# Kernel tuning notes

Measured on AMD Instinct MI355X. Metric: run time of the kernel, lower is better.

## Reference

```python
import jax, jax.numpy as jnp
import numpy as np
from jax import lax

FEAT = 384        # features
FFN = 768         # ffn_features (chunk=True -> halves of 384)
ZDIM = FFN // 2   # 384
HID = 192         # AE hidden
B, N = 4, 128
LN_EPS = 1e-5


def gelu(x):
    return jax.nn.gelu(x, approximate=False)  # torch nn.GELU default = exact erf


def setup_inputs() -> dict:
    key = jax.random.key(0)
    ks = jax.random.split(key, 12)

    def lin(k, fan_in, shape):
        bound = 1.0 / np.sqrt(fan_in)
        return jax.random.uniform(k, shape, jnp.float32, -bound, bound)

    return {
        "x": jax.random.normal(ks[0], (B, N, FEAT), jnp.float32),
        "U_w": lin(ks[1], FEAT, (FEAT, FFN)),
        "U_b": lin(ks[2], FEAT, (FFN,)),
        "ln_w": jnp.ones((ZDIM,), jnp.float32),
        "ln_b": jnp.zeros((ZDIM,), jnp.float32),
        "enc_w": lin(ks[3], ZDIM, (ZDIM, HID)),
        "enc_b": lin(ks[4], ZDIM, (HID,)),
        "dec_w": lin(ks[5], HID, (HID, ZDIM)),
        "dec_b": lin(ks[6], HID, (ZDIM,)),
        "V_w": lin(ks[7], ZDIM, (ZDIM, FEAT)),
        "V_b": lin(ks[8], ZDIM, (FEAT,)),
    }


def _ae(z, enc_w, enc_b, dec_w, dec_b):
    h = gelu(z @ enc_w + enc_b)
    return h @ dec_w + dec_b


def reference(x, U_w, U_b, ln_w, ln_b, enc_w, enc_b, dec_w, dec_b, V_w, V_b):
    h = gelu(x @ U_w + U_b)                    # (B,N,FFN)
    xh, z = jnp.split(h, 2, axis=-1)           # chunk=True: (B,N,ZDIM) each
    z = lax.stop_gradient(z)                   # z.detach()
    mu = jnp.mean(z, axis=-1, keepdims=True)
    var = jnp.var(z, axis=-1, keepdims=True)
    z = (z - mu) / jnp.sqrt(var + LN_EPS) * ln_w + ln_b

    n = z.shape[1]
    eye = jnp.eye(n, dtype=z.dtype)
    # z_mask[b,i,j,:] = z[b,j,:] if i==j else 0   (mask_type='zeros')
    z_mask = eye[None, :, :, None] * z[:, None, :, :]   # (B,N,N,ZDIM)
    preds = _ae(z_mask, enc_w, enc_b, dec_w, dec_b)      # (B,N,N,ZDIM)
    dist = jnp.einsum('bijf,bjf->bij', preds, z)         # (B,N,N)
    attn = lax.stop_gradient(jax.nn.softmax(dist, axis=-1))
    out = jnp.einsum('bij,bjf->bif', attn, xh)           # (B,N,ZDIM)
    return out @ V_w + V_b                               # (B,N,FEAT)
```

## Files before the change

### kernel.cpp

```cpp
#include <hip/hip_runtime.h>
#include <hip/hip_bf16.h>
#include <math.h>

#define FEAT 384
#define FFN  768
#define ZDIM 384
#define HID  192
#define BB   4
#define NN   128
#define BN   (BB*NN)

__device__ __forceinline__ float gelu_exact(float x) {
    return 0.5f * x * (1.0f + erff(x * 0.70710678118654752440f));
}

__device__ __forceinline__ float bflo(unsigned u) { return __uint_as_float(u << 16); }
__device__ __forceinline__ float bfhi(unsigned u) { return __uint_as_float(u & 0xFFFF0000u); }

template<bool F32>
__device__ __forceinline__ float ldg(const void* p, int i) {
    if constexpr (F32) return ((const float*)p)[i];
    return __uint_as_float(((unsigned)((const unsigned short*)p)[i]) << 16);
}

__device__ __forceinline__ unsigned pack2(float a, float b) {
    __hip_bfloat16 ba = __float2bfloat16(a), bb = __float2bfloat16(b);
    unsigned short ua, ub;
    __builtin_memcpy(&ua, &ba, 2);
    __builtin_memcpy(&ub, &bb, 2);
    return (unsigned)ua | ((unsigned)ub << 16);
}

template<bool F32>
__device__ __forceinline__ void st8(void* p, size_t off, const float v[8]) {
    if constexpr (F32) {
        *(float4*)((float*)p + off)     = make_float4(v[0], v[1], v[2], v[3]);
        *(float4*)((float*)p + off + 4) = make_float4(v[4], v[5], v[6], v[7]);
    } else {
        uint4 u;
        u.x = pack2(v[0], v[1]); u.y = pack2(v[2], v[3]);
        u.z = pack2(v[4], v[5]); u.w = pack2(v[6], v[7]);
        *(uint4*)((unsigned short*)p + off) = u;
    }
}

template<bool F32> struct V8;
template<> struct V8<true> {
    float4 a, b;
    __device__ __forceinline__ void load(const void* p, size_t off) {
        a = *(const float4*)((const float*)p + off);
        b = *(const float4*)((const float*)p + off + 4);
    }
    __device__ __forceinline__ float g(int i) const {
        return (i < 4) ? (&a.x)[i] : (&b.x)[i - 4];
    }
};
template<> struct V8<false> {
    uint4 u;
    __device__ __forceinline__ void load(const void* p, size_t off) {
        u = *(const uint4*)((const unsigned short*)p + off);
    }
    __device__ __forceinline__ float g(int i) const {
        const unsigned w = (&u.x)[i >> 1];
        return (i & 1) ? bfhi(w) : bflo(w);
    }
};
template<bool F32> struct V4;
template<> struct V4<true> {
    float4 a;
    __device__ __forceinline__ void load(const void* p, size_t off) {
        a = *(const float4*)((const float*)p + off);
    }
    __device__ __forceinline__ float g(int i) const { return (&a.x)[i]; }
};
template<> struct V4<false> {
    uint2 u;
    __device__ __forceinline__ void load(const void* p, size_t off) {
        u = *(const uint2*)((const unsigned short*)p + off);
    }
    __device__ __forceinline__ float g(int i) const {
        const unsigned w = (&u.x)[i >> 1];
        return (i & 1) ? bfhi(w) : bflo(w);
    }
};

__device__ __forceinline__ bool is_f32(const void* ln_w) {
    return ((const unsigned short*)ln_w)[0] == 0;
}

__device__ __forceinline__ float block_sum(float v, float* sm) {
    for (int o = 32; o > 0; o >>= 1) v += __shfl_down(v, o, 64);
    const int lane = threadIdx.x & 63, w = threadIdx.x >> 6;
    __syncthreads();
    if (lane == 0) sm[w] = v;
    __syncthreads();
    return sm[0] + sm[1] + sm[2] + sm[3] + sm[4] + sm[5];
}
__device__ __forceinline__ float2 block_sum2(float vx, float vy, float* sm) {
    for (int o = 32; o > 0; o >>= 1) {
        vx += __shfl_down(vx, o, 64);
        vy += __shfl_down(vy, o, 64);
    }
    const int lane = threadIdx.x & 63, w = threadIdx.x >> 6;
    __syncthreads();
    if (lane == 0) { sm[w] = vx; sm[w + 6] = vy; }
    __syncthreads();
    return make_float2(sm[0] + sm[1] + sm[2] + sm[3] + sm[4] + sm[5],
                       sm[6] + sm[7] + sm[8] + sm[9] + sm[10] + sm[11]);
}
__device__ __forceinline__ float block_max(float v, float* sm) {
    for (int o = 32; o > 0; o >>= 1) v = fmaxf(v, __shfl_down(v, o, 64));
    const int lane = threadIdx.x & 63, w = threadIdx.x >> 6;
    __syncthreads();
    if (lane == 0) sm[w] = v;
    __syncthreads();
    return fmaxf(fmaxf(fmaxf(sm[0], sm[1]), fmaxf(sm[2], sm[3])), fmaxf(sm[4], sm[5]));
}

template<bool F32>
__device__ void rows_body(
    const void* __restrict__ x, const void* __restrict__ U_w,
    const void* __restrict__ U_b, const void* __restrict__ ln_w,
    const void* __restrict__ ln_b, const void* __restrict__ enc_w,
    const void* __restrict__ enc_b, const void* __restrict__ dec_w,
    const void* __restrict__ dec_b,
    float* __restrict__ xh, float* __restrict__ d0, float* __restrict__ diag)
{
    const int r0 = 2 * blockIdx.x, r1 = r0 + 1;
    const int t = threadIdx.x;
    __shared__ float xs[2][FEAT];
    __shared__ float zs[2][ZDIM];
    __shared__ float hid[2][HID];
    __shared__ float gh[HID];
    __shared__ float part[4608];
    __shared__ float sm[12];

    xs[0][t] = ldg<F32>(x, r0 * FEAT + t);
    xs[1][t] = ldg<F32>(x, r1 * FEAT + t);
    if (t < HID) gh[t] = gelu_exact(ldg<F32>(enc_b, t));
    __syncthreads();

    const int cg = t % 96, kh = t / 96;
    const int cU = 8 * cg;
    const int kb = 96 * kh;
    float acc0[8] = {0,0,0,0,0,0,0,0}, acc1[8] = {0,0,0,0,0,0,0,0};
    {
        V8<F32> wa[8], wb[8];
        #pragma unroll
        for (int j = 0; j < 8; j++) wa[j].load(U_w, (size_t)(kb + j) * FFN + cU);
        for (int k0 = kb; k0 < kb + 96; k0 += 16) {
            #pragma unroll
            for (int j = 0; j < 8; j++) wb[j].load(U_w, (size_t)(k0 + 8 + j) * FFN + cU);
            #pragma unroll
            for (int j = 0; j < 8; j++) {
                const float x0 = xs[0][k0 + j], x1 = xs[1][k0 + j];
                #pragma unroll
                for (int i = 0; i < 8; i++) {
                    const float w = wa[j].g(i);
                    acc0[i] = fmaf(x0, w, acc0[i]);
                    acc1[i] = fmaf(x1, w, acc1[i]);
                }
            }
            if (k0 + 16 < kb + 96) {
                #pragma unroll
                for (int j = 0; j < 8; j++) wa[j].load(U_w, (size_t)(k0 + 16 + j) * FFN + cU);
            }
            #pragma unroll
            for (int j = 0; j < 8; j++) {
                const float x0 = xs[0][k0 + 8 + j], x1 = xs[1][k0 + 8 + j];
                #pragma unroll
                for (int i = 0; i < 8; i++) {
                    const float w = wb[j].g(i);
                    acc0[i] = fmaf(x0, w, acc0[i]);
                    acc1[i] = fmaf(x1, w, acc1[i]);
                }
            }
        }
    }
    if (kh > 0) {
        float* p = &part[(kh - 1) * 1536 + cg];
        #pragma unroll
        for (int i = 0; i < 8; i++) { p[i * 96] = acc0[i]; p[768 + i * 96] = acc1[i]; }
    }
    __syncthreads();

    float h0[8], h1[8];
    float s1a = 0.f, s1b = 0.f, s2a = 0.f, s2b = 0.f;
    if (kh == 0) {
        #pragma unroll
        for (int i = 0; i < 8; i++) {
            const float ub = ldg<F32>(U_b, cU + i);
            float v0 = acc0[i] + ub, v1 = acc1[i] + ub;
            #pragma unroll
            for (int kk = 0; kk < 3; kk++) {
                v0 += part[kk * 1536 + i * 96 + cg];
                v1 += part[kk * 1536 + 768 + i * 96 + cg];
            }
            v0 = gelu_exact(v0); v1 = gelu_exact(v1);
            h0[i] = v0; h1[i] = v1;
            if (cg >= 48) { s1a += v0; s2a += v0 * v0; s1b += v1; s2b += v1 * v1; }
        }
        if (cg < 48) {
            *(float4*)(xh + (size_t)r0 * ZDIM + cU)     = make_float4(h0[0], h0[1], h0[2], h0[3]);
            *(float4*)(xh + (size_t)r0 * ZDIM + cU + 4) = make_float4(h0[4], h0[5], h0[6], h0[7]);
            *(float4*)(xh + (size_t)r1 * ZDIM + cU)     = make_float4(h1[0], h1[1], h1[2], h1[3]);
            *(float4*)(xh + (size_t)r1 * ZDIM + cU + 4) = make_float4(h1[4], h1[5], h1[6], h1[7]);
        }
    }

    const float2 S1 = block_sum2(s1a, s1b, sm);
    const float2 S2 = block_sum2(s2a, s2b, sm);
    const float mu0 = S1.x * (1.0f / ZDIM), mu1 = S1.y * (1.0f / ZDIM);
    const float rs0 = rsqrtf(S2.x * (1.0f / ZDIM) - mu0 * mu0 + 1e-5f);
    const float rs1 = rsqrtf(S2.y * (1.0f / ZDIM) - mu1 * mu1 + 1e-5f);
    if (kh == 0 && cg >= 48) {
        #pragma unroll
        for (int i = 0; i < 8; i++) {
            const int zc = cU - ZDIM + i;
            const float w = ldg<F32>(ln_w, zc), bb = ldg<F32>(ln_b, zc);
            zs[0][zc] = (h0[i] - mu0) * rs0 * w + bb;
            zs[1][zc] = (h1[i] - mu1) * rs1 * w + bb;
        }
    }
    __syncthreads();

    {
        const int cgE = t % 48, khE = t / 48;
        const int cE = 4 * cgE, kbE = 48 * khE;
        float e0a[4] = {0,0,0,0}, e1a[4] = {0,0,0,0};
        V4<F32> va[8], vb[8];
        #pragma unroll
        for (int j = 0; j < 8; j++) va[j].load(enc_w, (size_t)(kbE + j) * HID + cE);
        for (int k0 = kbE; k0 < kbE + 48; k0 += 16) {
            #pragma unroll
            for (int j = 0; j < 8; j++) vb[j].load(enc_w, (size_t)(k0 + 8 + j) * HID + cE);
            #pragma unroll
            for (int j = 0; j < 8; j++) {
                const float z0 = zs[0][k0 + j], z1 = zs[1][k0 + j];
                #pragma unroll
                for (int i = 0; i < 4; i++) {
                    const float w = va[j].g(i);
                    e0a[i] = fmaf(z0, w, e0a[i]);
                    e1a[i] = fmaf(z1, w, e1a[i]);
                }
            }
            if (k0 + 16 < kbE + 48) {
                #pragma unroll
                for (int j = 0; j < 8; j++) va[j].load(enc_w, (size_t)(k0 + 16 + j) * HID + cE);
            }
            #pragma unroll
            for (int j = 0; j < 8; j++) {
                const float z0 = zs[0][k0 + 8 + j], z1 = zs[1][k0 + 8 + j];
                #pragma unroll
                for (int i = 0; i < 4; i++) {
                    const float w = vb[j].g(i);
                    e0a[i] = fmaf(z0, w, e0a[i]);
                    e1a[i] = fmaf(z1, w, e1a[i]);
                }
            }
        }
        if (khE > 0) {
            float* p = &part[(khE - 1) * 384 + cgE];
            #pragma unroll
            for (int i = 0; i < 4; i++) { p[i * 48] = e0a[i]; p[192 + i * 48] = e1a[i]; }
        }
        __syncthreads();
        if (khE == 0) {
            #pragma unroll
            for (int i = 0; i < 4; i++) {
                const float ebv = ldg<F32>(enc_b, cE + i);
                float v0 = e0a[i] + ebv, v1 = e1a[i] + ebv;
                #pragma unroll
                for (int kk = 0; kk < 7; kk++) {
                    v0 += part[kk * 384 + i * 48 + cgE];
                    v1 += part[kk * 384 + 192 + i * 48 + cgE];
                }
                hid[0][cE + i] = gelu_exact(v0);
                hid[1][cE + i] = gelu_exact(v1);
            }
        }
        __syncthreads();
    }

    {
        const int cgD = t % 96, khD = t / 96;
        const int cD = 4 * cgD, kbD = 48 * khD;
        float aa[4] = {0,0,0,0}, ab_[4] = {0,0,0,0}, ac[4] = {0,0,0,0};
        V4<F32> va[8], vb[8];
        #pragma unroll
        for (int j = 0; j < 8; j++) va[j].load(dec_w, (size_t)(kbD + j) * ZDIM + cD);
        for (int k0 = kbD; k0 < kbD + 48; k0 += 16) {
            #pragma unroll
            for (int j = 0; j < 8; j++) vb[j].load(dec_w, (size_t)(k0 + 8 + j) * ZDIM + cD);
            #pragma unroll
            for (int j = 0; j < 8; j++) {
                const float v0 = hid[0][k0 + j], v1 = hid[1][k0 + j], gv = gh[k0 + j];
                #pragma unroll
                for (int i = 0; i < 4; i++) {
                    const float w = va[j].g(i);
                    aa[i] = fmaf(v0, w, aa[i]);
                    ab_[i] = fmaf(v1, w, ab_[i]);
                    ac[i] = fmaf(gv, w, ac[i]);
                }
            }
            if (k0 + 16 < kbD + 48) {
                #pragma unroll
                for (int j = 0; j < 8; j++) va[j].load(dec_w, (size_t)(k0 + 16 + j) * ZDIM + cD);
            }
            #pragma unroll
            for (int j = 0; j < 8; j++) {
                const float v0 = hid[0][k0 + 8 + j], v1 = hid[1][k0 + 8 + j], gv = gh[k0 + 8 + j];
                #pragma unroll
                for (int i = 0; i < 4; i++) {
                    const float w = vb[j].g(i);
                    aa[i] = fmaf(v0, w, aa[i]);
                    ab_[i] = fmaf(v1, w, ab_[i]);
                    ac[i] = fmaf(gv, w, ac[i]);
                }
            }
        }
        if (khD > 0) {
            float* p = &part[(khD - 1) * 1152 + cgD];
            #pragma unroll
            for (int i = 0; i < 4; i++) {
                p[i * 96] = aa[i];
                p[384 + i * 96] = ab_[i];
                p[768 + i * 96] = ac[i];
            }
        }
        __syncthreads();
        float pd0 = 0.f, pd1 = 0.f, pe0 = 0.f, pe1 = 0.f;
        if (khD == 0) {
            #pragma unroll
            for (int i = 0; i < 4; i++) {
                const int c = cD + i;
                const float dbv = ldg<F32>(dec_b, c);
                float v0 = aa[i] + dbv, v1 = ab_[i] + dbv, v2 = ac[i] + dbv;
                #pragma unroll
                for (int kk = 0; kk < 3; kk++) {
                    v0 += part[kk * 1152 + i * 96 + cgD];
                    v1 += part[kk * 1152 + 384 + i * 96 + cgD];
                    v2 += part[kk * 1152 + 768 + i * 96 + cgD];
                }
                const float z0 = zs[0][c], z1 = zs[1][c];
                pd0 = fmaf(v0, z0, pd0);
                pd1 = fmaf(v1, z1, pd1);
                pe0 = fmaf(v2, z0, pe0);
                pe1 = fmaf(v2, z1, pe1);
            }
        }
        const float2 DG = block_sum2(pd0, pd1, sm);
        const float2 DD = block_sum2(pe0, pe1, sm);
        if (t == 0) {
            diag[r0] = DG.x; diag[r1] = DG.y;
            d0[r0] = DD.x;   d0[r1] = DD.y;
        }
    }
}

__global__ __launch_bounds__(384) void k_rows(
    const void* x, const void* U_w, const void* U_b,
    const void* ln_w, const void* ln_b,
    const void* enc_w, const void* enc_b,
    const void* dec_w, const void* dec_b,
    float* xh, float* d0, float* diag)
{
    if (is_f32(ln_w))
        rows_body<true >(x, U_w, U_b, ln_w, ln_b, enc_w, enc_b, dec_w, dec_b, xh, d0, diag);
    else
        rows_body<false>(x, U_w, U_b, ln_w, ln_b, enc_w, enc_b, dec_w, dec_b, xh, d0, diag);
}

template<bool F32>
__device__ void out_body(
    const float* __restrict__ d0, const float* __restrict__ diag,
    const float* __restrict__ xh,
    const void* __restrict__ V_w, const void* __restrict__ V_b,
    void* __restrict__ out)
{
    const int r0 = 2 * blockIdx.x, r1 = r0 + 1;
    const int b = r0 >> 7;
    const int t = threadIdx.x;
    __shared__ float e0s[NN];
    __shared__ float as[2][ZDIM];
    __shared__ float pv[5376];
    __shared__ float sm[12];

    float d0v = -INFINITY, dgv = -INFINITY;
    if (t < NN) { d0v = d0[b * NN + t]; dgv = diag[b * NN + t]; }
    const float m = block_max(fmaxf(d0v, dgv), sm);
    float e0v = 0.f;
    if (t < NN) { e0v = expf(d0v - m); e0s[t] = e0v; }
    const float S = block_sum(e0v, sm);

    const float e00 = expf(d0[r0] - m), e01 = expf(d0[r1] - m);
    const float ed0 = expf(diag[r0] - m), ed1 = expf(diag[r1] - m);
    const float inv0 = 1.0f / (S - e00 + ed0);
    const float inv1 = 1.0f / (S - e01 + ed1);

    float acc = 0.f;
    {
        const float* xp = xh + (size_t)b * NN * ZDIM + t;
        float wa[16], wb[16];
        #pragma unroll
        for (int j = 0; j < 16; j++) wa[j] = xp[(size_t)j * ZDIM];
        for (int j0 = 0; j0 < NN; j0 += 32) {
            #pragma unroll
            for (int j = 0; j < 16; j++) wb[j] = xp[(size_t)(j0 + 16 + j) * ZDIM];
            #pragma unroll
            for (int j = 0; j < 16; j++) acc = fmaf(e0s[j0 + j], wa[j], acc);
            if (j0 + 32 < NN) {
                #pragma unroll
                for (int j = 0; j < 16; j++) wa[j] = xp[(size_t)(j0 + 32 + j) * ZDIM];
            }
            #pragma unroll
            for (int j = 0; j < 16; j++) acc = fmaf(e0s[j0 + 16 + j], wb[j], acc);
        }
    }
    as[0][t] = (acc + (ed0 - e00) * xh[(size_t)r0 * ZDIM + t]) * inv0;
    as[1][t] = (acc + (ed1 - e01) * xh[(size_t)r1 * ZDIM + t]) * inv1;
    __syncthreads();

    const int cg = t % 48, kh = t / 48;
    const int cV = 8 * cg, kb = 48 * kh;
    float a0[8] = {0,0,0,0,0,0,0,0}, a1[8] = {0,0,0,0,0,0,0,0};
    {
        V8<F32> va[8], vb[8];
        #pragma unroll
        for (int j = 0; j < 8; j++) va[j].load(V_w, (size_t)(kb + j) * FEAT + cV);
        for (int f0 = kb; f0 < kb + 48; f0 += 16) {
            #pragma unroll
            for (int j = 0; j < 8; j++) vb[j].load(V_w, (size_t)(f0 + 8 + j) * FEAT + cV);
            #pragma unroll
            for (int j = 0; j < 8; j++) {
                const float s0 = as[0][f0 + j], s1 = as[1][f0 + j];
                #pragma unroll
                for (int i = 0; i < 8; i++) {
                    const float w = va[j].g(i);
                    a0[i] = fmaf(s0, w, a0[i]);
                    a1[i] = fmaf(s1, w, a1[i]);
                }
            }
            if (f0 + 16 < kb + 48) {
                #pragma unroll
                for (int j = 0; j < 8; j++) va[j].load(V_w, (size_t)(f0 + 16 + j) * FEAT + cV);
            }
            #pragma unroll
            for (int j = 0; j < 8; j++) {
                const float s0 = as[0][f0 + 8 + j], s1 = as[1][f0 + 8 + j];
                #pragma unroll
                for (int i = 0; i < 8; i++) {
                    const float w = vb[j].g(i);
                    a0[i] = fmaf(s0, w, a0[i]);
                    a1[i] = fmaf(s1, w, a1[i]);
                }
            }
        }
    }
    if (kh > 0) {
        float* p = &pv[(kh - 1) * 768 + cg];
        #pragma unroll
        for (int i = 0; i < 8; i++) { p[i * 48] = a0[i]; p[384 + i * 48] = a1[i]; }
    }
    __syncthreads();
    if (kh == 0) {
        float o0[8], o1[8];
        #pragma unroll
        for (int i = 0; i < 8; i++) {
            const float vb_ = ldg<F32>(V_b, cV + i);
            float u0 = a0[i] + vb_, u1 = a1[i] + vb_;
            #pragma unroll
            for (int kk = 0; kk < 7; kk++) {
                u0 += pv[kk * 768 + i * 48 + cg];
                u1 += pv[kk * 768 + 384 + i * 48 + cg];
            }
            o0[i] = u0; o1[i] = u1;
        }
        st8<F32>(out, (size_t)r0 * FEAT + cV, o0);
        st8<F32>(out, (size_t)r1 * FEAT + cV, o1);
    }
}

__global__ __launch_bounds__(384) void k_out(
    const void* ln_w,
    const float* d0, const float* diag, const float* xh,
    const void* V_w, const void* V_b, void* out)
{
    if (is_f32(ln_w))
        out_body<true >(d0, diag, xh, V_w, V_b, out);
    else
        out_body<false>(d0, diag, xh, V_w, V_b, out);
}

extern "C" void kernel_launch(void* const* d_in, const int* in_sizes, int n_in,
                              void* d_out, int out_size, void* d_ws, size_t ws_size,
                              hipStream_t stream) {
    const void* x     = d_in[0];
    const void* U_w   = d_in[1];
    const void* U_b   = d_in[2];
    const void* ln_w  = d_in[3];
    const void* ln_b  = d_in[4];
    const void* enc_w = d_in[5];
    const void* enc_b = d_in[6];
    const void* dec_w = d_in[7];
    const void* dec_b = d_in[8];
    const void* V_w   = d_in[9];
    const void* V_b   = d_in[10];

    float* ws   = (float*)d_ws;
    float* xh   = ws;
    float* d0   = xh + (size_t)BN * ZDIM;
    float* diag = d0 + BN;

    k_rows<<<BN / 2, 384, 0, stream>>>(x, U_w, U_b, ln_w, ln_b, enc_w, enc_b,
                                       dec_w, dec_b, xh, d0, diag);
    k_out<<<BN / 2, 384, 0, stream>>>(ln_w, d0, diag, xh, V_w, V_b, d_out);
}
```

Baseline: 111.2 us.

## Apply V projection to xh before attention and split row blocks by FFN half

Because out = attn·xh·V_w and the attention here is a rank-structured softmax (a shared baseline plus a diagonal correction), the V_w projection is moved ahead of attention. Each token's xh is projected to Y = xh·V_w inside the rows kernel, and the final kernel only forms the per-batch weighted sum of Y and applies the per-row diagonal correction. The rows kernel now launches two blocks per row pair: one computes the xh half and the Y projection, the other the z half with layernorm and the autoencoder. This raises parallelism and removes the per-row-pair V_w GEMM from the second kernel. The combine kernel runs only 16 blocks, which may leave most of the GPU idle, and the bf16 output now uses scalar stores.

```diff
diff --git a/kernel.cpp b/kernel.cpp
--- a/kernel.cpp
+++ b/kernel.cpp
@@ -22,26 +22,10 @@
     if constexpr (F32) return ((const float*)p)[i];
     return __uint_as_float(((unsigned)((const unsigned short*)p)[i]) << 16);
 }
-
-__device__ __forceinline__ unsigned pack2(float a, float b) {
-    __hip_bfloat16 ba = __float2bfloat16(a), bb = __float2bfloat16(b);
-    unsigned short ua, ub;
-    __builtin_memcpy(&ua, &ba, 2);
-    __builtin_memcpy(&ub, &bb, 2);
-    return (unsigned)ua | ((unsigned)ub << 16);
-}
-
 template<bool F32>
-__device__ __forceinline__ void st8(void* p, size_t off, const float v[8]) {
-    if constexpr (F32) {
-        *(float4*)((float*)p + off)     = make_float4(v[0], v[1], v[2], v[3]);
-        *(float4*)((float*)p + off + 4) = make_float4(v[4], v[5], v[6], v[7]);
-    } else {
-        uint4 u;
-        u.x = pack2(v[0], v[1]); u.y = pack2(v[2], v[3]);
-        u.z = pack2(v[4], v[5]); u.w = pack2(v[6], v[7]);
-        *(uint4*)((unsigned short*)p + off) = u;
-    }
+__device__ __forceinline__ void stg(void* p, size_t i, float v) {
+    if constexpr (F32) ((float*)p)[i] = v;
+    else ((__hip_bfloat16*)p)[i] = __float2bfloat16(v);
 }
 
 template<bool F32> struct V8;
@@ -123,47 +107,50 @@
     const void* __restrict__ U_b, const void* __restrict__ ln_w,
     const void* __restrict__ ln_b, const void* __restrict__ enc_w,
     const void* __restrict__ enc_b, const void* __restrict__ dec_w,
-    const void* __restrict__ dec_b,
-    float* __restrict__ xh, float* __restrict__ d0, float* __restrict__ diag)
+    const void* __restrict__ dec_b, const void* __restrict__ V_w,
+    float* __restrict__ Y, float* __restrict__ d0, float* __restrict__ diag)
 {
-    const int r0 = 2 * blockIdx.x, r1 = r0 + 1;
+    const int pr = blockIdx.x >> 1;
+    const int h  = blockIdx.x & 1;
+    const int r0 = 2 * pr, r1 = r0 + 1;
     const int t = threadIdx.x;
     __shared__ float xs[2][FEAT];
     __shared__ float zs[2][ZDIM];
     __shared__ float hid[2][HID];
     __shared__ float gh[HID];
-    __shared__ float part[4608];
+    __shared__ float part[5376];
     __shared__ float sm[12];
 
     xs[0][t] = ldg<F32>(x, r0 * FEAT + t);
     xs[1][t] = ldg<F32>(x, r1 * FEAT + t);
-    if (t < HID) gh[t] = gelu_exact(ldg<F32>(enc_b, t));
-    __syncthreads();
-
-    const int cg = t % 96, kh = t / 96;
-    const int cU = 8 * cg;
-    const int kb = 96 * kh;
-    float acc0[8] = {0,0,0,0,0,0,0,0}, acc1[8] = {0,0,0,0,0,0,0,0};
+    if (h && t < HID) gh[t] = gelu_exact(ldg<F32>(enc_b, t));
+    __syncthreads();
+
+    const int cg = t % 48, kh = t / 48;
+    const int cL = 8 * cg;
+    const int cG = 384 * h + cL;
+    const int kb = 48 * kh;
+    float a0[8] = {0,0,0,0,0,0,0,0}, a1[8] = {0,0,0,0,0,0,0,0};
     {
         V8<F32> wa[8], wb[8];
         #pragma unroll
-        for (int j = 0; j < 8; j++) wa[j].load(U_w, (size_t)(kb + j) * FFN + cU);
-        for (int k0 = kb; k0 < kb + 96; k0 += 16) {
-            #pragma unroll
-            for (int j = 0; j < 8; j++) wb[j].load(U_w, (size_t)(k0 + 8 + j) * FFN + cU);
+        for (int j = 0; j < 8; j++) wa[j].load(U_w, (size_t)(kb + j) * FFN + cG);
+        for (int k0 = kb; k0 < kb + 48; k0 += 16) {
+            #pragma unroll
+            for (int j = 0; j < 8; j++) wb[j].load(U_w, (size_t)(k0 + 8 + j) * FFN + cG);
             #pragma unroll
             for (int j = 0; j < 8; j++) {
                 const float x0 = xs[0][k0 + j], x1 = xs[1][k0 + j];
                 #pragma unroll
                 for (int i = 0; i < 8; i++) {
                     const float w = wa[j].g(i);
-                    acc0[i] = fmaf(x0, w, acc0[i]);
-                    acc1[i] = fmaf(x1, w, acc1[i]);
-                }
-            }
-            if (k0 + 16 < kb + 96) {
-                #pragma unroll
-                for (int j = 0; j < 8; j++) wa[j].load(U_w, (size_t)(k0 + 16 + j) * FFN + cU);
+                    a0[i] = fmaf(x0, w, a0[i]);
+                    a1[i] = fmaf(x1, w, a1[i]);
+                }
+            }
+            if (k0 + 16 < kb + 48) {
+                #pragma unroll
+                for (int j = 0; j < 8; j++) wa[j].load(U_w, (size_t)(k0 + 16 + j) * FFN + cG);
             }
             #pragma unroll
             for (int j = 0; j < 8; j++) {
@@ -171,52 +158,118 @@
                 #pragma unroll
                 for (int i = 0; i < 8; i++) {
                     const float w = wb[j].g(i);
-                    acc0[i] = fmaf(x0, w, acc0[i]);
-                    acc1[i] = fmaf(x1, w, acc1[i]);
+                    a0[i] = fmaf(x0, w, a0[i]);
+                    a1[i] = fmaf(x1, w, a1[i]);
                 }
             }
         }
     }
     if (kh > 0) {
-        float* p = &part[(kh - 1) * 1536 + cg];
-        #pragma unroll
-        for (int i = 0; i < 8; i++) { p[i * 96] = acc0[i]; p[768 + i * 96] = acc1[i]; }
+        float* p = &part[(kh - 1) * 768 + cg];
+        #pragma unroll
+        for (int i = 0; i < 8; i++) { p[i * 48] = a0[i]; p[384 + i * 48] = a1[i]; }
     }
     __syncthreads();
 
     float h0[8], h1[8];
+    if (kh == 0) {
+        #pragma unroll
+        for (int i = 0; i < 8; i++) {
+            const float ub = ldg<F32>(U_b, cG + i);
+            float v0 = a0[i] + ub, v1 = a1[i] + ub;
+            #pragma unroll
+            for (int kk = 0; kk < 7; kk++) {
+                v0 += part[kk * 768 + i * 48 + cg];
+                v1 += part[kk * 768 + 384 + i * 48 + cg];
+            }
+            h0[i] = gelu_exact(v0);
+            h1[i] = gelu_exact(v1);
+        }
+    }
+
+    if (h == 0) {
+        if (kh == 0) {
+            #pragma unroll
+            for (int i = 0; i < 8; i++) { zs[0][cL + i] = h0[i]; zs[1][cL + i] = h1[i]; }
+        }
+        __syncthreads();
+        float y0[8] = {0,0,0,0,0,0,0,0}, y1[8] = {0,0,0,0,0,0,0,0};
+        {
+            V8<F32> va[8], vb[8];
+            #pragma unroll
+            for (int j = 0; j < 8; j++) va[j].load(V_w, (size_t)(kb + j) * FEAT + cL);
+            for (int k0 = kb; k0 < kb + 48; k0 += 16) {
+                #pragma unroll
+                for (int j = 0; j < 8; j++) vb[j].load(V_w, (size_t)(k0 + 8 + j) * FEAT + cL);
+                #pragma unroll
+                for (int j = 0; j < 8; j++) {
+                    const float s0 = zs[0][k0 + j], s1 = zs[1][k0 + j];
+                    #pragma unroll
+                    for (int i = 0; i < 8; i++) {
+                        const float w = va[j].g(i);
+                        y0[i] = fmaf(s0, w, y0[i]);
+                        y1[i] = fmaf(s1, w, y1[i]);
+                    }
+                }
+                if (k0 + 16 < kb + 48) {
+                    #pragma unroll
+                    for (int j = 0; j < 8; j++) va[j].load(V_w, (size_t)(k0 + 16 + j) * FEAT + cL);
+                }
+                #pragma unroll
+                for (int j = 0; j < 8; j++) {
+                    const float s0 = zs[0][k0 + 8 + j], s1 = zs[1][k0 + 8 + j];
+                    #pragma unroll
+                    for (int i = 0; i < 8; i++) {
+                        const float w = vb[j].g(i);
+                        y0[i] = fmaf(s0, w, y0[i]);
+                        y1[i] = fmaf(s1, w, y1[i]);
+                    }
+                }
+            }
+        }
+        if (kh > 0) {
+            float* p = &part[(kh - 1) * 768 + cg];
+            #pragma unroll
+            for (int i = 0; i < 8; i++) { p[i * 48] = y0[i]; p[384 + i * 48] = y1[i]; }
+        }
+        __syncthreads();
+        if (kh == 0) {
+            float o0[8], o1[8];
+            #pragma unroll
+            for (int i = 0; i < 8; i++) {
+                float u0 = y0[i], u1 = y1[i];
+                #pragma unroll
+                for (int kk = 0; kk < 7; kk++) {
+                    u0 += part[kk * 768 + i * 48 + cg];
+                    u1 += part[kk * 768 + 384 + i * 48 + cg];
+                }
+                o0[i] = u0; o1[i] = u1;
+            }
+            *(float4*)(Y + (size_t)r0 * FEAT + cL)     = make_float4(o0[0], o0[1], o0[2], o0[3]);
+            *(float4*)(Y + (size_t)r0 * FEAT + cL + 4) = make_float4(o0[4], o0[5], o0[6], o0[7]);
+            *(float4*)(Y + (size_t)r1 * FEAT + cL)     = make_float4(o1[0], o1[1], o1[2], o1[3]);
+            *(float4*)(Y + (size_t)r1 * FEAT + cL + 4) = make_float4(o1[4], o1[5], o1[6], o1[7]);
+        }
+        return;
+    }
+
     float s1a = 0.f, s1b = 0.f, s2a = 0.f, s2b = 0.f;
     if (kh == 0) {
         #pragma unroll
         for (int i = 0; i < 8; i++) {
-            const float ub = ldg<F32>(U_b, cU + i);
-            float v0 = acc0[i] + ub, v1 = acc1[i] + ub;
-            #pragma unroll
-            for (int kk = 0; kk < 3; kk++) {
-                v0 += part[kk * 1536 + i * 96 + cg];
-                v1 += part[kk * 1536 + 768 + i * 96 + cg];
-            }
-            v0 = gelu_exact(v0); v1 = gelu_exact(v1);
-            h0[i] = v0; h1[i] = v1;
-            if (cg >= 48) { s1a += v0; s2a += v0 * v0; s1b += v1; s2b += v1 * v1; }
-        }
-        if (cg < 48) {
-            *(float4*)(xh + (size_t)r0 * ZDIM + cU)     = make_float4(h0[0], h0[1], h0[2], h0[3]);
-            *(float4*)(xh + (size_t)r0 * ZDIM + cU + 4) = make_float4(h0[4], h0[5], h0[6], h0[7]);
-            *(float4*)(xh + (size_t)r1 * ZDIM + cU)     = make_float4(h1[0], h1[1], h1[2], h1[3]);
-            *(float4*)(xh + (size_t)r1 * ZDIM + cU + 4) = make_float4(h1[4], h1[5], h1[6], h1[7]);
-        }
-    }
-
+            s1a += h0[i]; s2a += h0[i] * h0[i];
+            s1b += h1[i]; s2b += h1[i] * h1[i];
+        }
+    }
     const float2 S1 = block_sum2(s1a, s1b, sm);
     const float2 S2 = block_sum2(s2a, s2b, sm);
     const float mu0 = S1.x * (1.0f / ZDIM), mu1 = S1.y * (1.0f / ZDIM);
     const float rs0 = rsqrtf(S2.x * (1.0f / ZDIM) - mu0 * mu0 + 1e-5f);
     const float rs1 = rsqrtf(S2.y * (1.0f / ZDIM) - mu1 * mu1 + 1e-5f);
-    if (kh == 0 && cg >= 48) {
+    if (kh == 0) {
         #pragma unroll
         for (int i = 0; i < 8; i++) {
-            const int zc = cU - ZDIM + i;
+            const int zc = cL + i;
             const float w = ldg<F32>(ln_w, zc), bb = ldg<F32>(ln_b, zc);
             zs[0][zc] = (h0[i] - mu0) * rs0 * w + bb;
             zs[1][zc] = (h1[i] - mu1) * rs1 * w + bb;
@@ -362,134 +415,81 @@
     const void* x, const void* U_w, const void* U_b,
     const void* ln_w, const void* ln_b,
     const void* enc_w, const void* enc_b,
-    const void* dec_w, const void* dec_b,
-    float* xh, float* d0, float* diag)
+    const void* dec_w, const void* dec_b, const void* V_w,
+    float* Y, float* d0, float* diag)
 {
     if (is_f32(ln_w))
-        rows_body<true >(x, U_w, U_b, ln_w, ln_b, enc_w, enc_b, dec_w, dec_b, xh, d0, diag);
+        rows_body<true >(x, U_w, U_b, ln_w, ln_b, enc_w, enc_b, dec_w, dec_b, V_w, Y, d0, diag);
     else
-        rows_body<false>(x, U_w, U_b, ln_w, ln_b, enc_w, enc_b, dec_w, dec_b, xh, d0, diag);
+        rows_body<false>(x, U_w, U_b, ln_w, ln_b, enc_w, enc_b, dec_w, dec_b, V_w, Y, d0, diag);
 }
 
 template<bool F32>
-__device__ void out_body(
+__device__ void combine_body(
     const float* __restrict__ d0, const float* __restrict__ diag,
-    const float* __restrict__ xh,
-    const void* __restrict__ V_w, const void* __restrict__ V_b,
-    void* __restrict__ out)
+    const float* __restrict__ Y,
+    const void* __restrict__ V_b, void* __restrict__ out)
 {
-    const int r0 = 2 * blockIdx.x, r1 = r0 + 1;
-    const int b = r0 >> 7;
+    const int b  = blockIdx.x >> 2;
+    const int cc = (blockIdx.x & 3) * 96;
     const int t = threadIdx.x;
-    __shared__ float e0s[NN];
-    __shared__ float as[2][ZDIM];
-    __shared__ float pv[5376];
+    const int c = t % 96, q = t / 96;
+    __shared__ float e0s[NN], eds[NN];
+    __shared__ float bp[4 * 96];
+    __shared__ float baseY[96];
     __shared__ float sm[12];
 
     float d0v = -INFINITY, dgv = -INFINITY;
     if (t < NN) { d0v = d0[b * NN + t]; dgv = diag[b * NN + t]; }
     const float m = block_max(fmaxf(d0v, dgv), sm);
     float e0v = 0.f;
-    if (t < NN) { e0v = expf(d0v - m); e0s[t] = e0v; }
+    if (t < NN) {
+        e0v = expf(d0v - m);
+        e0s[t] = e0v;
+        eds[t] = expf(dgv - m);
+    }
     const float S = block_sum(e0v, sm);
 
-    const float e00 = expf(d0[r0] - m), e01 = expf(d0[r1] - m);
-    const float ed0 = expf(diag[r0] - m), ed1 = expf(diag[r1] - m);
-    const float inv0 = 1.0f / (S - e00 + ed0);
-    const float inv1 = 1.0f / (S - e01 + ed1);
-
-    float acc = 0.f;
-    {
-        const float* xp = xh + (size_t)b * NN * ZDIM + t;
-        float wa[16], wb[16];
-        #pragma unroll
-        for (int j = 0; j < 16; j++) wa[j] = xp[(size_t)j * ZDIM];
-        for (int j0 = 0; j0 < NN; j0 += 32) {
-            #pragma unroll
-            for (int j = 0; j < 16; j++) wb[j] = xp[(size_t)(j0 + 16 + j) * ZDIM];
-            #pragma unroll
-            for (int j = 0; j < 16; j++) acc = fmaf(e0s[j0 + j], wa[j], acc);
-            if (j0 + 32 < NN) {
-                #pragma unroll
-                for (int j = 0; j < 16; j++) wa[j] = xp[(size_t)(j0 + 32 + j) * ZDIM];
-            }
-            #pragma unroll
-            for (int j = 0; j < 16; j++) acc = fmaf(e0s[j0 + 16 + j], wb[j], acc);
-        }
-    }
-    as[0][t] = (acc + (ed0 - e00) * xh[(size_t)r0 * ZDIM + t]) * inv0;
-    as[1][t] = (acc + (ed1 - e01) * xh[(size_t)r1 * ZDIM + t]) * inv1;
-    __syncthreads();
-
-    const int cg = t % 48, kh = t / 48;
-    const int cV = 8 * cg, kb = 48 * kh;
-    float a0[8] = {0,0,0,0,0,0,0,0}, a1[8] = {0,0,0,0,0,0,0,0};
-    {
-        V8<F32> va[8], vb[8];
-        #pragma unroll
-        for (int j = 0; j < 8; j++) va[j].load(V_w, (size_t)(kb + j) * FEAT + cV);
-        for (int f0 = kb; f0 < kb + 48; f0 += 16) {
-            #pragma unroll
-            for (int j = 0; j < 8; j++) vb[j].load(V_w, (size_t)(f0 + 8 + j) * FEAT + cV);
-            #pragma unroll
-            for (int j = 0; j < 8; j++) {
-                const float s0 = as[0][f0 + j], s1 = as[1][f0 + j];
-                #pragma unroll
-                for (int i = 0; i < 8; i++) {
-                    const float w = va[j].g(i);
-                    a0[i] = fmaf(s0, w, a0[i]);
-                    a1[i] = fmaf(s1, w, a1[i]);
-                }
-            }
-            if (f0 + 16 < kb + 48) {
-                #pragma unroll
-                for (int j = 0; j < 8; j++) va[j].load(V_w, (size_t)(f0 + 16 + j) * FEAT + cV);
-            }
-            #pragma unroll
-            for (int j = 0; j < 8; j++) {
-                const float s0 = as[0][f0 + 8 + j], s1 = as[1][f0 + 8 + j];
-                #pragma unroll
-                for (int i = 0; i < 8; i++) {
-                    const float w = vb[j].g(i);
-                    a0[i] = fmaf(s0, w, a0[i]);
-                    a1[i] = fmaf(s1, w, a1[i]);
-                }
-            }
-        }
-    }
-    if (kh > 0) {
-        float* p = &pv[(kh - 1) * 768 + cg];
-        #pragma unroll
-        for (int i = 0; i < 8; i++) { p[i * 48] = a0[i]; p[384 + i * 48] = a1[i]; }
-    }
-    __syncthreads();
-    if (kh == 0) {
-        float o0[8], o1[8];
-        #pragma unroll
-        for (int i = 0; i < 8; i++) {
-            const float vb_ = ldg<F32>(V_b, cV + i);
-            float u0 = a0[i] + vb_, u1 = a1[i] + vb_;
-            #pragma unroll
-            for (int kk = 0; kk < 7; kk++) {
-                u0 += pv[kk * 768 + i * 48 + cg];
-                u1 += pv[kk * 768 + 384 + i * 48 + cg];
-            }
-            o0[i] = u0; o1[i] = u1;
-        }
-        st8<F32>(out, (size_t)r0 * FEAT + cV, o0);
-        st8<F32>(out, (size_t)r1 * FEAT + cV, o1);
-    }
-}
-
-__global__ __launch_bounds__(384) void k_out(
+    const float* Yb = Y + (size_t)b * NN * FEAT + cc + c;
+    const int j0 = 32 * q;
+    float p = 0.f;
+    for (int jj = 0; jj < 32; jj += 8) {
+        float w[8];
+        #pragma unroll
+        for (int j = 0; j < 8; j++) w[j] = Yb[(size_t)(j0 + jj + j) * FEAT];
+        #pragma unroll
+        for (int j = 0; j < 8; j++) p = fmaf(e0s[j0 + jj + j], w[j], p);
+    }
+    bp[q * 96 + c] = p;
+    __syncthreads();
+    if (q == 0) baseY[c] = bp[c] + bp[96 + c] + bp[192 + c] + bp[288 + c];
+    __syncthreads();
+
+    const float bY = baseY[c];
+    const float vb = ldg<F32>(V_b, cc + c);
+    for (int rr = 0; rr < 32; rr += 8) {
+        float w[8];
+        #pragma unroll
+        for (int j = 0; j < 8; j++) w[j] = Yb[(size_t)(j0 + rr + j) * FEAT];
+        #pragma unroll
+        for (int j = 0; j < 8; j++) {
+            const int r = j0 + rr + j;
+            const float inv = 1.0f / (S - e0s[r] + eds[r]);
+            const float val = (bY + (eds[r] - e0s[r]) * w[j]) * inv + vb;
+            stg<F32>(out, (size_t)(b * NN + r) * FEAT + cc + c, val);
+        }
+    }
+}
+
+__global__ __launch_bounds__(384) void k_combine(
     const void* ln_w,
-    const float* d0, const float* diag, const float* xh,
-    const void* V_w, const void* V_b, void* out)
+    const float* d0, const float* diag, const float* Y,
+    const void* V_b, void* out)
 {
     if (is_f32(ln_w))
-        out_body<true >(d0, diag, xh, V_w, V_b, out);
+        combine_body<true >(d0, diag, Y, V_b, out);
     else
-        out_body<false>(d0, diag, xh, V_w, V_b, out);
+        combine_body<false>(d0, diag, Y, V_b, out);
 }
 
 extern "C" void kernel_launch(void* const* d_in, const int* in_sizes, int n_in,
@@ -508,11 +508,11 @@
     const void* V_b   = d_in[10];
 
     float* ws   = (float*)d_ws;
-    float* xh   = ws;
-    float* d0   = xh + (size_t)BN * ZDIM;
+    float* Y    = ws;
+    float* d0   = Y + (size_t)BN * FEAT;
     float* diag = d0 + BN;
 
-    k_rows<<<BN / 2, 384, 0, stream>>>(x, U_w, U_b, ln_w, ln_b, enc_w, enc_b,
-                                       dec_w, dec_b, xh, d0, diag);
-    k_out<<<BN / 2, 384, 0, stream>>>(ln_w, d0, diag, xh, V_w, V_b, d_out);
-}
+    k_rows<<<BN, 384, 0, stream>>>(x, U_w, U_b, ln_w, ln_b, enc_w, enc_b,
+                                   dec_w, dec_b, V_w, Y, d0, diag);
+    k_combine<<<4 * BB, 384, 0, stream>>>(ln_w, d0, diag, Y, V_b, d_out);
+}
```

Result: slower. 117.6 us (+5.7%).
